# Kernel tuning notes

Hardware: AMD Instinct MI355X
Metric: run time of the kernel (lower is better)

## Reference

```python
import jax, jax.numpy as jnp
import numpy as np

N_NODES = 100000
N_EDGES = 1600000
IN_DIM = 128
HID_DIM = 128
OUT_DIM = 2


def sage_conv(x, src, dst, deg_inv, W_l, W_r, b):
    # mean-aggregate neighbor features: messages flow src -> dst
    agg = jax.ops.segment_sum(x[src], dst, num_segments=N_NODES)  # [N, d_in]
    agg = agg * deg_inv[:, None]
    # PyG SAGEConv: out = lin_l(aggr) + lin_r(x); bias only on lin_l
    return agg @ W_l + x @ W_r + b


def setup_inputs() -> dict:
    key = jax.random.key(0)
    ks = jax.random.split(key, 9)
    x = jax.random.normal(ks[0], (N_NODES, IN_DIM), dtype=jnp.float32)
    edge_index = jax.random.randint(ks[1], (2, N_EDGES), 0, N_NODES, dtype=jnp.int64)

    def glorot(k, shape):
        lim = float(np.sqrt(6.0 / (shape[0] + shape[1])))
        return jax.random.uniform(k, shape, jnp.float32, -lim, lim)

    return {
        "x": x,
        "edge_index": edge_index,
        "W1_l": glorot(ks[2], (IN_DIM, HID_DIM)),
        "W1_r": glorot(ks[3], (IN_DIM, HID_DIM)),
        "b1": jnp.zeros((HID_DIM,), jnp.float32),
        "W2_l": glorot(ks[4], (HID_DIM, HID_DIM)),
        "W2_r": glorot(ks[5], (HID_DIM, HID_DIM)),
        "b2": jnp.zeros((HID_DIM,), jnp.float32),
        "W3_l": glorot(ks[6], (HID_DIM, OUT_DIM)),
        "W3_r": glorot(ks[7], (HID_DIM, OUT_DIM)),
        "b3": jnp.zeros((OUT_DIM,), jnp.float32),
    }


def reference(x, edge_index, W1_l, W1_r, b1, W2_l, W2_r, b2, W3_l, W3_r, b3):
    src, dst = edge_index[0], edge_index[1]
    # mean-aggregation normalization: 1/in-degree (clamped to >=1)
    deg = jax.ops.segment_sum(jnp.ones((N_EDGES,), jnp.float32), dst, num_segments=N_NODES)
    deg_inv = 1.0 / jnp.maximum(deg, 1.0)

    h = sage_conv(x, src, dst, deg_inv, W1_l, W1_r, b1)
    h = jax.nn.relu(h)  # dropout is identity in eval mode
    h = sage_conv(h, src, dst, deg_inv, W2_l, W2_r, b2)
    h = jax.nn.relu(h)
    h = sage_conv(h, src, dst, deg_inv, W3_l, W3_r, b3)
    h = jax.nn.relu(h)
    return jax.nn.log_softmax(h, axis=1)
```

## Files before the change

### kernel.cpp

```cpp
#include <hip/hip_runtime.h>
#include <math.h>

#define DIM 128

typedef __attribute__((ext_vector_type(8))) short bf16x8;
typedef __attribute__((ext_vector_type(4))) float f32x4;

__device__ __forceinline__ ushort f2bf(float f) {
  unsigned u = __float_as_uint(f);
  return (ushort)((u + 0x7FFFu + ((u >> 16) & 1u)) >> 16);
}
__device__ __forceinline__ float bf2f(ushort h) {
  return __uint_as_float(((unsigned)h) << 16);
}


__global__ __launch_bounds__(256) void count_cast_kernel(
    const int* __restrict__ dst, unsigned* __restrict__ counts, int E, int NB, int NBUCK,
    const float* __restrict__ x, ushort* __restrict__ xh, long total_f,
    const float* __restrict__ W1l, const float* __restrict__ W1r,
    const float* __restrict__ W2l, const float* __restrict__ W2r,
    ushort* __restrict__ tabs, int CB) {
  __shared__ unsigned hist[1024];
  const int tid = threadIdx.x;
  int bid = blockIdx.x;
  if (bid < NB) {
    for (int i = tid; i < NBUCK; i += 256) hist[i] = 0u;
    __syncthreads();
    long base = (long)bid * 2048;
#pragma unroll
    for (int c = 0; c < 8; ++c) {
      long e = base + c * 256 + tid;
      if (e < E) atomicAdd(&hist[((unsigned)dst[e]) >> 7], 1u);
    }
    __syncthreads();
    for (int i = tid; i < NBUCK; i += 256)
      counts[(size_t)bid * NBUCK + i] = hist[i];
    return;
  }
  int aid = bid - NB;
  if (aid < CB) {
    long i = ((long)aid * 2048 + tid) * 4;
    for (int c = 0; c < 8; ++c, i += 1024) {
      if (i >= total_f) break;
      float4 v = *(const float4*)(x + i);
      uint2 Hh;
      Hh.x = (unsigned)f2bf(v.x) | ((unsigned)f2bf(v.y) << 16);
      Hh.y = (unsigned)f2bf(v.z) | ((unsigned)f2bf(v.w) << 16);
      *(uint2*)(xh + i) = Hh;
    }
    return;
  }
  int aid2 = aid - CB;
  if (aid2 < 256) {
    int m = aid2 >> 6;
    const float* W = (m == 0) ? W1l : (m == 1) ? W1r : (m == 2) ? W2l : W2r;
    ushort* Ht = tabs + (size_t)m * 16384;
    int idx = (aid2 & 63) * 256 + tid;
    int k = idx >> 7, n = idx & 127;
    Ht[n * DIM + k] = f2bf(W[idx]);
  }
}

__global__ __launch_bounds__(256) void colscan_kernel(unsigned* __restrict__ counts,
                                                      unsigned* __restrict__ totals,
                                                      int NB, int NBUCK) {
  int wid = (blockIdx.x << 2) + (threadIdx.x >> 6);
  int lane = threadIdx.x & 63;
  if (wid >= NBUCK) return;
  unsigned carry = 0u;
  for (int k0 = 0; k0 < NB; k0 += 64) {
    int k = k0 + lane;
    unsigned v = (k < NB) ? counts[(size_t)k * NBUCK + wid] : 0u;
    unsigned s = v;
#pragma unroll
    for (int o = 1; o < 64; o <<= 1) {
      unsigned t = __shfl_up(s, o, 64);
      if (lane >= o) s += t;
    }
    if (k < NB) counts[(size_t)k * NBUCK + wid] = carry + s - v;
    carry += __shfl(s, 63, 64);
  }
  if (lane == 0) totals[wid] = carry;
}

__global__ __launch_bounds__(256) void totscan_kernel(unsigned* __restrict__ totals,
                                                      int NBUCK, int E) {
  __shared__ unsigned s[256];
  __shared__ unsigned carry;
  if (threadIdx.x == 0) carry = 0u;
  __syncthreads();
  for (int base = 0; base < NBUCK; base += 256) {
    int i = base + threadIdx.x;
    unsigned v = (i < NBUCK) ? totals[i] : 0u;
    s[threadIdx.x] = v;
    __syncthreads();
#pragma unroll
    for (int d = 1; d < 256; d <<= 1) {
      unsigned t = (threadIdx.x >= d) ? s[threadIdx.x - d] : 0u;
      __syncthreads();
      s[threadIdx.x] += t;
      __syncthreads();
    }
    if (i < NBUCK) totals[i] = carry + s[threadIdx.x] - v;
    __syncthreads();
    if (threadIdx.x == 0) carry += s[255];
    __syncthreads();
  }
  if (threadIdx.x == 0) totals[NBUCK] = (unsigned)E;
}

__global__ __launch_bounds__(256) void cscatter_kernel(
    const int* __restrict__ src, const int* __restrict__ dst,
    const unsigned* __restrict__ counts, const unsigned* __restrict__ totals,
    uint2* __restrict__ pairs, int E, int NBUCK) {
  __shared__ unsigned basec[1024];
  const int tid = threadIdx.x;
  const int bid = blockIdx.x;
  for (int i = tid; i < NBUCK; i += 256)
    basec[i] = counts[(size_t)bid * NBUCK + i] + totals[i];
  __syncthreads();
  long base = (long)bid * 2048;
#pragma unroll
  for (int c = 0; c < 8; ++c) {
    long e = base + c * 256 + tid;
    if (e < E) {
      int d = dst[e];
      unsigned pos = atomicAdd(&basec[((unsigned)d) >> 7], 1u);
      pairs[pos] = make_uint2((unsigned)src[e], (unsigned)d);
    }
  }
}

__global__ __launch_bounds__(256) void fine_kernel(
    const uint2* __restrict__ pairs, const unsigned* __restrict__ totals,
    int* __restrict__ csr_src, unsigned* __restrict__ offs, float* __restrict__ dinv,
    int N, int NBUCK, int E) {
  __shared__ int lsrc[4096];
  __shared__ ushort ldst[4096];
  __shared__ unsigned hist[128], excl[128], cur[128];
  const int tid = threadIdx.x;
  const int b = blockIdx.x;
  const unsigned t0 = totals[b], t1 = totals[b + 1];
  unsigned cnt = t1 - t0;
  if (cnt > 4096u) cnt = 4096u;
  if (tid < 128) { hist[tid] = 0u; cur[tid] = 0u; }
  __syncthreads();
  for (unsigned i = tid; i < cnt; i += 256) {
    uint2 p = pairs[t0 + i];
    lsrc[i] = (int)p.x;
    int nl = (int)(p.y & 127u);
    ldst[i] = (ushort)nl;
    atomicAdd(&hist[nl], 1u);
  }
  __syncthreads();
  if (tid < 64) {
    unsigned v0 = hist[tid], v1 = hist[tid + 64];
    unsigned s0 = v0, s1 = v1;
#pragma unroll
    for (int o = 1; o < 64; o <<= 1) {
      unsigned u0 = __shfl_up(s0, o, 64);
      unsigned u1 = __shfl_up(s1, o, 64);
      if (tid >= o) { s0 += u0; s1 += u1; }
    }
    unsigned tot0 = __shfl(s0, 63, 64);
    excl[tid] = s0 - v0;
    excl[tid + 64] = tot0 + s1 - v1;
  }
  __syncthreads();
  if (tid < 128) {
    int node = (b << 7) + tid;
    if (node < N) {
      offs[node] = t0 + excl[tid];
      dinv[node] = 1.0f / fmaxf((float)hist[tid], 1.0f);
    }
  }
  if (b == 0 && tid == 255) offs[N] = (unsigned)E;
  for (unsigned i = tid; i < cnt; i += 256) {
    int nl = (int)ldst[i];
    unsigned slot = excl[nl] + atomicAdd(&cur[nl], 1u);
    csr_src[t0 + slot] = lsrc[i];
  }
}


#define GATHER_BODY(TABLE)                                                       \
  const int node = (blockIdx.x * 256 + threadIdx.x) >> 6;                        \
  if (node >= N) return;                                                         \
  const int lane = threadIdx.x & 63;                                             \
  const int eslot = lane >> 4;                                                   \
  const int col = lane & 15;                                                     \
  const unsigned beg = off[node], end = off[node + 1];                           \
  const ushort* fbase = (TABLE) + col * 8;                                       \
  float acc[8];                                                                  \
  _Pragma("unroll") for (int t = 0; t < 8; ++t) acc[t] = 0.f;                    \
  auto accum = [&](int4 v) {                                                     \
    unsigned w0 = (unsigned)v.x, w1 = (unsigned)v.y;                             \
    unsigned w2 = (unsigned)v.z, w3 = (unsigned)v.w;                             \
    acc[0] += __uint_as_float(w0 << 16);                                         \
    acc[1] += __uint_as_float(w0 & 0xFFFF0000u);                                 \
    acc[2] += __uint_as_float(w1 << 16);                                         \
    acc[3] += __uint_as_float(w1 & 0xFFFF0000u);                                 \
    acc[4] += __uint_as_float(w2 << 16);                                         \
    acc[5] += __uint_as_float(w2 & 0xFFFF0000u);                                 \
    acc[6] += __uint_as_float(w3 << 16);                                         \
    acc[7] += __uint_as_float(w3 & 0xFFFF0000u);                                 \
  };                                                                             \
  unsigned base = beg;                                                           \
  for (; base + 16 <= end; base += 16) {                                         \
    int s0 = csr_src[base + eslot];                                              \
    int s1 = csr_src[base + 4 + eslot];                                          \
    int s2 = csr_src[base + 8 + eslot];                                          \
    int s3 = csr_src[base + 12 + eslot];                                         \
    int4 v0 = *(const int4*)(fbase + (size_t)s0 * DIM);                          \
    int4 v1 = *(const int4*)(fbase + (size_t)s1 * DIM);                          \
    int4 v2 = *(const int4*)(fbase + (size_t)s2 * DIM);                          \
    int4 v3 = *(const int4*)(fbase + (size_t)s3 * DIM);                          \
    accum(v0); accum(v1); accum(v2); accum(v3);                                  \
  }                                                                              \
  for (; base + 8 <= end; base += 8) {                                           \
    int s0 = csr_src[base + eslot];                                              \
    int s1 = csr_src[base + 4 + eslot];                                          \
    int4 v0 = *(const int4*)(fbase + (size_t)s0 * DIM);                          \
    int4 v1 = *(const int4*)(fbase + (size_t)s1 * DIM);                          \
    accum(v0); accum(v1);                                                        \
  }                                                                              \
  for (unsigned e = base + eslot; e < end; e += 4) {                             \
    int s = csr_src[e];                                                          \
    int4 v = *(const int4*)(fbase + (size_t)s * DIM);                            \
    accum(v);                                                                    \
  }                                                                              \
  _Pragma("unroll") for (int t = 0; t < 8; ++t) {                                \
    acc[t] += __shfl_xor(acc[t], 32, 64);                                        \
    acc[t] += __shfl_xor(acc[t], 16, 64);                                        \
  }

__global__ __launch_bounds__(256) void gather_wave_kernel(
    const ushort* __restrict__ featH, const int* __restrict__ csr_src,
    const unsigned* __restrict__ off, const float* __restrict__ dinv,
    ushort* __restrict__ aggH, int N) {
  GATHER_BODY(featH)
  if (eslot == 0) {
    float di = dinv[node];
    unsigned ph[4];
#pragma unroll
    for (int t = 0; t < 4; ++t) {
      ph[t] = (unsigned)f2bf(acc[2 * t] * di) | ((unsigned)f2bf(acc[2 * t + 1] * di) << 16);
    }
    *(int4*)(aggH + (size_t)node * DIM + col * 8) =
        make_int4((int)ph[0], (int)ph[1], (int)ph[2], (int)ph[3]);
  }
}

__global__ __launch_bounds__(256) void sage_mfma_kernel(
    const ushort* __restrict__ aggH, const ushort* xH,
    const ushort* __restrict__ WlH, const ushort* __restrict__ WrH,
    const float* __restrict__ bias,
    const float* __restrict__ W3l, const float* __restrict__ W3r,
    ushort* __restrict__ outH, float* __restrict__ y, int N) {
  __shared__ ushort As[128 * 64];
  __shared__ ushort Bs[128 * 64];

  const int tid = threadIdx.x;
  const int bm = blockIdx.x * 128;
  const int wave = tid >> 6;
  const int lane = tid & 63;
  const int l15 = lane & 15;
  const int quad = lane >> 4;
  const int wm = wave >> 1;
  const int wn = wave & 1;

  f32x4 acc[4][4];
#pragma unroll
  for (int i = 0; i < 4; ++i)
#pragma unroll
    for (int j = 0; j < 4; ++j) acc[i][j] = (f32x4){0.f, 0.f, 0.f, 0.f};

  for (int g = 0; g < 4; ++g) {
    const ushort* Ap = (g < 2) ? aggH : xH;
    const ushort* Wp = (g < 2) ? WlH : WrH;
    const int kt = (g & 1) << 6;
    __syncthreads();
#pragma unroll
    for (int c = 0; c < 4; ++c) {
      int flat = c * 256 + tid;
      int row = flat >> 3;
      int kg = flat & 7;
      int swz = (kg ^ (row & 7)) << 3;
      int grow = bm + row;
      if (grow >= N) grow = N - 1;
      *(int4*)(&As[row * 64 + swz]) = *(const int4*)(Ap + (size_t)grow * DIM + kt + kg * 8);
      *(int4*)(&Bs[row * 64 + swz]) = *(const int4*)(Wp + (size_t)row * DIM + kt + kg * 8);
    }
    __syncthreads();
#pragma unroll
    for (int ks = 0; ks < 2; ++ks) {
      bf16x8 af[4], bfr[4];
      int kg = (ks << 2) + quad;
#pragma unroll
      for (int i = 0; i < 4; ++i) {
        int ar = (wm << 6) + (i << 4) + l15;
        af[i] = *(const bf16x8*)(&As[ar * 64 + ((kg ^ (ar & 7)) << 3)]);
        int br = (wn << 6) + (i << 4) + l15;
        bfr[i] = *(const bf16x8*)(&Bs[br * 64 + ((kg ^ (br & 7)) << 3)]);
      }
#pragma unroll
      for (int i = 0; i < 4; ++i)
#pragma unroll
        for (int j = 0; j < 4; ++j)
          acc[i][j] = __builtin_amdgcn_mfma_f32_16x16x32_bf16(af[i], bfr[j], acc[i][j], 0, 0, 0);
    }
  }

  __syncthreads();
  float* WcF = reinterpret_cast<float*>(As);
  float* YpF = reinterpret_cast<float*>(As) + 512;

  if (W3l) {
    for (int t = tid; t < 512; t += 256) {
      int col = t >> 2, c = t & 3;
      WcF[t] = (c < 2) ? W3l[col * 2 + c] : W3r[col * 2 + (c - 2)];
    }
    __syncthreads();
  }

  float bv[4];
#pragma unroll
  for (int j = 0; j < 4; ++j) bv[j] = bias[(wn << 6) + (j << 4) + l15];

#pragma unroll
  for (int i = 0; i < 4; ++i) {
#pragma unroll
    for (int r = 0; r < 4; ++r) {
      const int rowl = (wm << 6) + (i << 4) + (quad << 2) + r;
      const int grow = bm + rowl;
      float p0 = 0.f, p1 = 0.f, p2 = 0.f, p3 = 0.f;
#pragma unroll
      for (int j = 0; j < 4; ++j) {
        int col = (wn << 6) + (j << 4) + l15;
        float v = fmaxf(acc[i][j][r] + bv[j], 0.f);
        ushort h = f2bf(v);
        if (outH && grow < N) outH[(size_t)grow * DIM + col] = h;
        if (W3l) {
          float qv = bf2f(h);
          p0 += qv * WcF[col * 4 + 0];
          p1 += qv * WcF[col * 4 + 1];
          p2 += qv * WcF[col * 4 + 2];
          p3 += qv * WcF[col * 4 + 3];
        }
      }
      if (W3l) {
#pragma unroll
        for (int o = 1; o < 16; o <<= 1) {
          p0 += __shfl_xor(p0, o, 64);
          p1 += __shfl_xor(p1, o, 64);
          p2 += __shfl_xor(p2, o, 64);
          p3 += __shfl_xor(p3, o, 64);
        }
        if (l15 == 0) {
          YpF[(rowl * 4 + 0) * 2 + wn] = p0;
          YpF[(rowl * 4 + 1) * 2 + wn] = p1;
          YpF[(rowl * 4 + 2) * 2 + wn] = p2;
          YpF[(rowl * 4 + 3) * 2 + wn] = p3;
        }
      }
    }
  }

  if (W3l) {
    __syncthreads();
    for (int t = tid; t < 512; t += 256) {
      int grow = bm + (t >> 2);
      if (grow < N) y[(size_t)grow * 4 + (t & 3)] = YpF[t * 2 + 0] + YpF[t * 2 + 1];
    }
  }
}

__global__ __launch_bounds__(256) void final3_kernel(const float* __restrict__ y,
                                                     const int* __restrict__ csr_src,
                                                     const unsigned* __restrict__ off,
                                                     const float* __restrict__ dinv,
                                                     const float* __restrict__ b3,
                                                     float* __restrict__ out, int N) {
  int n = blockIdx.x * 256 + threadIdx.x;
  if (n >= N) return;
  unsigned beg = off[n], end = off[n + 1];
  float s0 = 0.f, s1 = 0.f;
  for (unsigned e = beg; e < end; ++e) {
    int s = csr_src[e];
    float2 v = *reinterpret_cast<const float2*>(&y[(size_t)s * 4]);
    s0 += v.x; s1 += v.y;
  }
  float di = dinv[n];
  float o0 = fmaxf(s0 * di + y[(size_t)n * 4 + 2] + b3[0], 0.f);
  float o1 = fmaxf(s1 * di + y[(size_t)n * 4 + 3] + b3[1], 0.f);
  float m = fmaxf(o0, o1);
  float l = m + logf(expf(o0 - m) + expf(o1 - m));
  out[n * 2 + 0] = o0 - l;
  out[n * 2 + 1] = o1 - l;
}

extern "C" void kernel_launch(void* const* d_in, const int* in_sizes, int n_in,
                              void* d_out, int out_size, void* d_ws, size_t ws_size,
                              hipStream_t stream) {
  const float* x   = (const float*)d_in[0];
  const int*   ei  = (const int*)d_in[1];
  const float* W1l = (const float*)d_in[2];
  const float* W1r = (const float*)d_in[3];
  const float* b1  = (const float*)d_in[4];
  const float* W2l = (const float*)d_in[5];
  const float* W2r = (const float*)d_in[6];
  const float* b2  = (const float*)d_in[7];
  const float* W3l = (const float*)d_in[8];
  const float* W3r = (const float*)d_in[9];
  const float* b3  = (const float*)d_in[10];

  const int N = in_sizes[0] / DIM;
  const int E = in_sizes[1] / 2;
  const int* src = ei;
  const int* dst = ei + E;

  const int NBUCK = (N + 127) >> 7;
  const int NB    = (E + 2047) / 2048;
  const long total_f = (long)N * DIM;
  const int CB    = (int)((total_f / 4 + 2047) / 2048);

  char* ws = (char*)d_ws;
  size_t off_b = 0;
  auto alloc = [&](size_t bytes) {
    void* p = ws + off_b;
    off_b = (off_b + bytes + 255) & ~(size_t)255;
    return p;
  };
  unsigned* counts  = (unsigned*)alloc((size_t)NB * NBUCK * 4);
  unsigned* totals  = (unsigned*)alloc((size_t)(NBUCK + 1) * 4);
  void*     shared_ = alloc((size_t)N * DIM * 2);
  uint2*    pairs   = (uint2*)shared_;
  ushort*   aggH    = (ushort*)shared_;
  int*      csr_src = (int*)alloc((size_t)E * 4);
  unsigned* offs    = (unsigned*)alloc((size_t)(N + 1) * 4);
  float*    dinv    = (float*)alloc((size_t)N * 4);
  ushort*   xh      = (ushort*)alloc((size_t)N * DIM * 2);
  ushort*   tabs    = (ushort*)alloc((size_t)4 * 16384 * 2);
  float*    y       = (float*)alloc((size_t)N * 4 * 4);

  count_cast_kernel<<<NB + CB + 256, 256, 0, stream>>>(
      dst, counts, E, NB, NBUCK, x, xh, total_f, W1l, W1r, W2l, W2r, tabs, CB);
  colscan_kernel<<<(NBUCK + 3) / 4, 256, 0, stream>>>(counts, totals, NB, NBUCK);
  totscan_kernel<<<1, 256, 0, stream>>>(totals, NBUCK, E);
  cscatter_kernel<<<NB, 256, 0, stream>>>(src, dst, counts, totals, pairs, E, NBUCK);
  fine_kernel<<<NBUCK, 256, 0, stream>>>(pairs, totals, csr_src, offs, dinv, N, NBUCK, E);

  const ushort* W1lH = tabs;
  const ushort* W1rH = tabs + 16384;
  const ushort* W2lH = tabs + 32768;
  const ushort* W2rH = tabs + 49152;
  const int G = (N + 127) / 128;
  const int gather_grid = (N + 3) / 4;

  gather_wave_kernel<<<gather_grid, 256, 0, stream>>>(xh, csr_src, offs, dinv, aggH, N);
  sage_mfma_kernel<<<G, 256, 0, stream>>>(aggH, xh, W1lH, W1rH, b1,
                                          nullptr, nullptr, xh, nullptr, N);
  gather_wave_kernel<<<gather_grid, 256, 0, stream>>>(xh, csr_src, offs, dinv, aggH, N);
  sage_mfma_kernel<<<G, 256, 0, stream>>>(aggH, xh, W2lH, W2rH, b2,
                                          W3l, W3r, nullptr, y, N);
  final3_kernel<<<(N + 255) / 256, 256, 0, stream>>>(y, csr_src, offs, dinv, b3, (float*)d_out, N);
}
```

Before: 360.4 us.

## Reorder layer-2 as transform-then-aggregate, fuse W3 projection into gather

Layer 2 now runs the GEMMs first: a dual-output MFMA kernel computes h@W2_l and h@W2_r+b2. A new gather kernel then aggregates the pre-transformed features, applies ReLU and projects onto W3, which removes the separate aggregate-then-GEMM pass and the W3 epilogue in the MFMA kernel. Edge pairs are also packed into 32 bits (src<<7 | local dst), and the gather tail is made branchless with clamped loads. The layer-1 MFMA epilogue now stages output through LDS so global stores are coalesced. The cost is an extra N×128 bf16 buffer and rounding h@W2_l to bf16 before aggregation, which slightly changes numerics.

```diff
diff --git a/kernel.cpp b/kernel.cpp
--- a/kernel.cpp
+++ b/kernel.cpp
@@ -113,7 +113,7 @@
 __global__ __launch_bounds__(256) void cscatter_kernel(
     const int* __restrict__ src, const int* __restrict__ dst,
     const unsigned* __restrict__ counts, const unsigned* __restrict__ totals,
-    uint2* __restrict__ pairs, int E, int NBUCK) {
+    unsigned* __restrict__ pairs, int E, int NBUCK) {
   __shared__ unsigned basec[1024];
   const int tid = threadIdx.x;
   const int bid = blockIdx.x;
@@ -125,15 +125,15 @@
   for (int c = 0; c < 8; ++c) {
     long e = base + c * 256 + tid;
     if (e < E) {
-      int d = dst[e];
-      unsigned pos = atomicAdd(&basec[((unsigned)d) >> 7], 1u);
-      pairs[pos] = make_uint2((unsigned)src[e], (unsigned)d);
+      unsigned d = (unsigned)dst[e];
+      unsigned pos = atomicAdd(&basec[d >> 7], 1u);
+      pairs[pos] = ((unsigned)src[e] << 7) | (d & 127u);
     }
   }
 }
 
 __global__ __launch_bounds__(256) void fine_kernel(
-    const uint2* __restrict__ pairs, const unsigned* __restrict__ totals,
+    const unsigned* __restrict__ pairs, const unsigned* __restrict__ totals,
     int* __restrict__ csr_src, unsigned* __restrict__ offs, float* __restrict__ dinv,
     int N, int NBUCK, int E) {
   __shared__ int lsrc[4096];
@@ -147,9 +147,9 @@
   if (tid < 128) { hist[tid] = 0u; cur[tid] = 0u; }
   __syncthreads();
   for (unsigned i = tid; i < cnt; i += 256) {
-    uint2 p = pairs[t0 + i];
-    lsrc[i] = (int)p.x;
-    int nl = (int)(p.y & 127u);
+    unsigned p = pairs[t0 + i];
+    lsrc[i] = (int)(p >> 7);
+    int nl = (int)(p & 127u);
     ldst[i] = (ushort)nl;
     atomicAdd(&hist[nl], 1u);
   }
@@ -218,17 +218,21 @@
     int4 v3 = *(const int4*)(fbase + (size_t)s3 * DIM);                          \
     accum(v0); accum(v1); accum(v2); accum(v3);                                  \
   }                                                                              \
-  for (; base + 8 <= end; base += 8) {                                           \
-    int s0 = csr_src[base + eslot];                                              \
-    int s1 = csr_src[base + 4 + eslot];                                          \
+  if (base < end) {                                                              \
+    unsigned e0 = base + eslot, e1 = base + 4 + eslot;                           \
+    unsigned e2 = base + 8 + eslot, e3 = base + 12 + eslot;                      \
+    int s0 = csr_src[e0 < end ? e0 : end - 1];                                   \
+    int s1 = csr_src[e1 < end ? e1 : end - 1];                                   \
+    int s2 = csr_src[e2 < end ? e2 : end - 1];                                   \
+    int s3 = csr_src[e3 < end ? e3 : end - 1];                                   \
     int4 v0 = *(const int4*)(fbase + (size_t)s0 * DIM);                          \
     int4 v1 = *(const int4*)(fbase + (size_t)s1 * DIM);                          \
-    accum(v0); accum(v1);                                                        \
-  }                                                                              \
-  for (unsigned e = base + eslot; e < end; e += 4) {                             \
-    int s = csr_src[e];                                                          \
-    int4 v = *(const int4*)(fbase + (size_t)s * DIM);                            \
-    accum(v);                                                                    \
+    int4 v2 = *(const int4*)(fbase + (size_t)s2 * DIM);                          \
+    int4 v3 = *(const int4*)(fbase + (size_t)s3 * DIM);                          \
+    if (e0 < end) accum(v0);                                                     \
+    if (e1 < end) accum(v1);                                                     \
+    if (e2 < end) accum(v2);                                                     \
+    if (e3 < end) accum(v3);                                                     \
   }                                                                              \
   _Pragma("unroll") for (int t = 0; t < 8; ++t) {                                \
     acc[t] += __shfl_xor(acc[t], 32, 64);                                        \
@@ -252,12 +256,52 @@
   }
 }
 
+__global__ __launch_bounds__(256) void gather2_kernel(
+    const ushort* __restrict__ h1l, const int* __restrict__ csr_src,
+    const unsigned* __restrict__ off, const float* __restrict__ dinv,
+    const ushort* __restrict__ h1r, const float* __restrict__ W3l,
+    const float* __restrict__ W3r, float* __restrict__ y, int N) {
+  GATHER_BODY(h1l)
+  if (eslot == 0) {
+    float di = dinv[node];
+    int4 xv = *(const int4*)(h1r + (size_t)node * DIM + col * 8);
+    unsigned w0 = (unsigned)xv.x, w1 = (unsigned)xv.y;
+    unsigned w2 = (unsigned)xv.z, w3 = (unsigned)xv.w;
+    float h[8];
+    h[0] = fmaxf(acc[0] * di + __uint_as_float(w0 << 16), 0.f);
+    h[1] = fmaxf(acc[1] * di + __uint_as_float(w0 & 0xFFFF0000u), 0.f);
+    h[2] = fmaxf(acc[2] * di + __uint_as_float(w1 << 16), 0.f);
+    h[3] = fmaxf(acc[3] * di + __uint_as_float(w1 & 0xFFFF0000u), 0.f);
+    h[4] = fmaxf(acc[4] * di + __uint_as_float(w2 << 16), 0.f);
+    h[5] = fmaxf(acc[5] * di + __uint_as_float(w2 & 0xFFFF0000u), 0.f);
+    h[6] = fmaxf(acc[6] * di + __uint_as_float(w3 << 16), 0.f);
+    h[7] = fmaxf(acc[7] * di + __uint_as_float(w3 & 0xFFFF0000u), 0.f);
+    const int d0 = col * 8;
+    float y0 = 0.f, y1 = 0.f, y2 = 0.f, y3 = 0.f;
+#pragma unroll
+    for (int t = 0; t < 8; t += 2) {
+      float4 wl = *(const float4*)(W3l + (size_t)(d0 + t) * 2);
+      float4 wr = *(const float4*)(W3r + (size_t)(d0 + t) * 2);
+      y0 += h[t] * wl.x + h[t + 1] * wl.z;
+      y1 += h[t] * wl.y + h[t + 1] * wl.w;
+      y2 += h[t] * wr.x + h[t + 1] * wr.z;
+      y3 += h[t] * wr.y + h[t + 1] * wr.w;
+    }
+#pragma unroll
+    for (int o = 1; o < 16; o <<= 1) {
+      y0 += __shfl_xor(y0, o, 64);
+      y1 += __shfl_xor(y1, o, 64);
+      y2 += __shfl_xor(y2, o, 64);
+      y3 += __shfl_xor(y3, o, 64);
+    }
+    if (lane == 0) *(float4*)(y + (size_t)node * 4) = make_float4(y0, y1, y2, y3);
+  }
+}
+
 __global__ __launch_bounds__(256) void sage_mfma_kernel(
     const ushort* __restrict__ aggH, const ushort* xH,
     const ushort* __restrict__ WlH, const ushort* __restrict__ WrH,
-    const float* __restrict__ bias,
-    const float* __restrict__ W3l, const float* __restrict__ W3r,
-    ushort* __restrict__ outH, float* __restrict__ y, int N) {
+    const float* __restrict__ bias, ushort* __restrict__ outH, int N) {
   __shared__ ushort As[128 * 64];
   __shared__ ushort Bs[128 * 64];
 
@@ -312,66 +356,125 @@
     }
   }
 
-  __syncthreads();
-  float* WcF = reinterpret_cast<float*>(As);
-  float* YpF = reinterpret_cast<float*>(As) + 512;
-
-  if (W3l) {
-    for (int t = tid; t < 512; t += 256) {
-      int col = t >> 2, c = t & 3;
-      WcF[t] = (c < 2) ? W3l[col * 2 + c] : W3r[col * 2 + (c - 2)];
-    }
-    __syncthreads();
-  }
-
   float bv[4];
 #pragma unroll
   for (int j = 0; j < 4; ++j) bv[j] = bias[(wn << 6) + (j << 4) + l15];
 
-#pragma unroll
-  for (int i = 0; i < 4; ++i) {
-#pragma unroll
-    for (int r = 0; r < 4; ++r) {
-      const int rowl = (wm << 6) + (i << 4) + (quad << 2) + r;
-      const int grow = bm + rowl;
-      float p0 = 0.f, p1 = 0.f, p2 = 0.f, p3 = 0.f;
-#pragma unroll
-      for (int j = 0; j < 4; ++j) {
-        int col = (wn << 6) + (j << 4) + l15;
-        float v = fmaxf(acc[i][j][r] + bv[j], 0.f);
-        ushort h = f2bf(v);
-        if (outH && grow < N) outH[(size_t)grow * DIM + col] = h;
-        if (W3l) {
-          float qv = bf2f(h);
-          p0 += qv * WcF[col * 4 + 0];
-          p1 += qv * WcF[col * 4 + 1];
-          p2 += qv * WcF[col * 4 + 2];
-          p3 += qv * WcF[col * 4 + 3];
+  __syncthreads();
+#pragma unroll
+  for (int i = 0; i < 4; ++i)
+#pragma unroll
+    for (int j = 0; j < 4; ++j)
+#pragma unroll
+      for (int r = 0; r < 4; ++r) {
+        int row = (wm << 6) + (i << 4) + (quad << 2) + r;
+        int colc = (wn << 6) + (j << 4) + l15;
+        ((ushort*)As)[((row & 63) << 7) + colc + ((row >> 6) << 13)] =
+            f2bf(fmaxf(acc[i][j][r] + bv[j], 0.f));
+      }
+  __syncthreads();
+#pragma unroll
+  for (int c = 0; c < 8; ++c) {
+    int flat = c * 256 + tid;
+    int row = flat >> 4;
+    int grow = bm + row;
+    if (grow < N)
+      *(int4*)(outH + (size_t)grow * DIM + (flat & 15) * 8) =
+          *(const int4*)((const ushort*)As + flat * 8);
+  }
+}
+
+__global__ __launch_bounds__(256) void gemm2_dual_kernel(
+    const ushort* __restrict__ h1, const ushort* __restrict__ tabs2,
+    const float* __restrict__ b2, ushort* __restrict__ h1l, ushort* __restrict__ h1r, int N) {
+  __shared__ ushort L[3 * 128 * 64];
+  ushort* As = L;
+  ushort* Bs0 = L + 8192;
+  ushort* Bs1 = L + 16384;
+  const int tid = threadIdx.x;
+  const int bm = blockIdx.x * 128;
+  const int wave = tid >> 6;
+  const int lane = tid & 63;
+  const int l15 = lane & 15;
+  const int quad = lane >> 4;
+  const int wm = wave >> 1;
+  const int wn = wave & 1;
+
+  f32x4 accl[4][4], accr[4][4];
+#pragma unroll
+  for (int i = 0; i < 4; ++i)
+#pragma unroll
+    for (int j = 0; j < 4; ++j) {
+      accl[i][j] = (f32x4){0.f, 0.f, 0.f, 0.f};
+      accr[i][j] = (f32x4){0.f, 0.f, 0.f, 0.f};
+    }
+
+  for (int g = 0; g < 2; ++g) {
+    const int kt = g << 6;
+    __syncthreads();
+#pragma unroll
+    for (int c = 0; c < 4; ++c) {
+      int flat = c * 256 + tid;
+      int row = flat >> 3;
+      int kg = flat & 7;
+      int swz = (kg ^ (row & 7)) << 3;
+      int grow = bm + row;
+      if (grow >= N) grow = N - 1;
+      *(int4*)(&As[row * 64 + swz]) = *(const int4*)(h1 + (size_t)grow * DIM + kt + kg * 8);
+      *(int4*)(&Bs0[row * 64 + swz]) = *(const int4*)(tabs2 + (size_t)row * DIM + kt + kg * 8);
+      *(int4*)(&Bs1[row * 64 + swz]) =
+          *(const int4*)(tabs2 + 16384 + (size_t)row * DIM + kt + kg * 8);
+    }
+    __syncthreads();
+#pragma unroll
+    for (int ks = 0; ks < 2; ++ks) {
+      bf16x8 af[4], bl[4], br[4];
+      int kg = (ks << 2) + quad;
+#pragma unroll
+      for (int i = 0; i < 4; ++i) {
+        int ar = (wm << 6) + (i << 4) + l15;
+        af[i] = *(const bf16x8*)(&As[ar * 64 + ((kg ^ (ar & 7)) << 3)]);
+        int nr = (wn << 6) + (i << 4) + l15;
+        bl[i] = *(const bf16x8*)(&Bs0[nr * 64 + ((kg ^ (nr & 7)) << 3)]);
+        br[i] = *(const bf16x8*)(&Bs1[nr * 64 + ((kg ^ (nr & 7)) << 3)]);
+      }
+#pragma unroll
+      for (int i = 0; i < 4; ++i)
+#pragma unroll
+        for (int j = 0; j < 4; ++j) {
+          accl[i][j] = __builtin_amdgcn_mfma_f32_16x16x32_bf16(af[i], bl[j], accl[i][j], 0, 0, 0);
+          accr[i][j] = __builtin_amdgcn_mfma_f32_16x16x32_bf16(af[i], br[j], accr[i][j], 0, 0, 0);
         }
-      }
-      if (W3l) {
-#pragma unroll
-        for (int o = 1; o < 16; o <<= 1) {
-          p0 += __shfl_xor(p0, o, 64);
-          p1 += __shfl_xor(p1, o, 64);
-          p2 += __shfl_xor(p2, o, 64);
-          p3 += __shfl_xor(p3, o, 64);
+    }
+  }
+
+  float bv[4];
+#pragma unroll
+  for (int j = 0; j < 4; ++j) bv[j] = b2[(wn << 6) + (j << 4) + l15];
+
+#pragma unroll
+  for (int m = 0; m < 2; ++m) {
+    __syncthreads();
+#pragma unroll
+    for (int i = 0; i < 4; ++i)
+#pragma unroll
+      for (int j = 0; j < 4; ++j)
+#pragma unroll
+        for (int r = 0; r < 4; ++r) {
+          int row = (wm << 6) + (i << 4) + (quad << 2) + r;
+          int colc = (wn << 6) + (j << 4) + l15;
+          float v = m ? (accr[i][j][r] + bv[j]) : accl[i][j][r];
+          L[row * 128 + colc] = f2bf(v);
         }
-        if (l15 == 0) {
-          YpF[(rowl * 4 + 0) * 2 + wn] = p0;
-          YpF[(rowl * 4 + 1) * 2 + wn] = p1;
-          YpF[(rowl * 4 + 2) * 2 + wn] = p2;
-          YpF[(rowl * 4 + 3) * 2 + wn] = p3;
-        }
-      }
-    }
-  }
-
-  if (W3l) {
-    __syncthreads();
-    for (int t = tid; t < 512; t += 256) {
-      int grow = bm + (t >> 2);
-      if (grow < N) y[(size_t)grow * 4 + (t & 3)] = YpF[t * 2 + 0] + YpF[t * 2 + 1];
+    __syncthreads();
+    ushort* out = m ? h1r : h1l;
+#pragma unroll
+    for (int c = 0; c < 8; ++c) {
+      int flat = c * 256 + tid;
+      int row = flat >> 4;
+      int grow = bm + row;
+      if (grow < N)
+        *(int4*)(out + (size_t)grow * DIM + (flat & 15) * 8) = *(const int4*)(&L[flat * 8]);
     }
   }
 }
@@ -435,14 +538,16 @@
   unsigned* counts  = (unsigned*)alloc((size_t)NB * NBUCK * 4);
   unsigned* totals  = (unsigned*)alloc((size_t)(NBUCK + 1) * 4);
   void*     shared_ = alloc((size_t)N * DIM * 2);
-  uint2*    pairs   = (uint2*)shared_;
+  unsigned* pairs   = (unsigned*)shared_;
   ushort*   aggH    = (ushort*)shared_;
+  ushort*   h1l     = (ushort*)shared_;
   int*      csr_src = (int*)alloc((size_t)E * 4);
   unsigned* offs    = (unsigned*)alloc((size_t)(N + 1) * 4);
   float*    dinv    = (float*)alloc((size_t)N * 4);
   ushort*   xh      = (ushort*)alloc((size_t)N * DIM * 2);
   ushort*   tabs    = (ushort*)alloc((size_t)4 * 16384 * 2);
   float*    y       = (float*)alloc((size_t)N * 4 * 4);
+  ushort*   h1r     = (ushort*)alloc((size_t)N * DIM * 2);
 
   count_cast_kernel<<<NB + CB + 256, 256, 0, stream>>>(
       dst, counts, E, NB, NBUCK, x, xh, total_f, W1l, W1r, W2l, W2r, tabs, CB);
@@ -453,16 +558,13 @@
 
   const ushort* W1lH = tabs;
   const ushort* W1rH = tabs + 16384;
-  const ushort* W2lH = tabs + 32768;
-  const ushort* W2rH = tabs + 49152;
+  const ushort* tabs2 = tabs + 32768;
   const int G = (N + 127) / 128;
   const int gather_grid = (N + 3) / 4;
 
   gather_wave_kernel<<<gather_grid, 256, 0, stream>>>(xh, csr_src, offs, dinv, aggH, N);
-  sage_mfma_kernel<<<G, 256, 0, stream>>>(aggH, xh, W1lH, W1rH, b1,
-                                          nullptr, nullptr, xh, nullptr, N);
-  gather_wave_kernel<<<gather_grid, 256, 0, stream>>>(xh, csr_src, offs, dinv, aggH, N);
-  sage_mfma_kernel<<<G, 256, 0, stream>>>(aggH, xh, W2lH, W2rH, b2,
-                                          W3l, W3r, nullptr, y, N);
+  sage_mfma_kernel<<<G, 256, 0, stream>>>(aggH, xh, W1lH, W1rH, b1, xh, N);
+  gemm2_dual_kernel<<<G, 256, 0, stream>>>(xh, tabs2, b2, h1l, h1r, N);
+  gather2_kernel<<<gather_grid, 256, 0, stream>>>(h1l, csr_src, offs, dinv, h1r, W3l, W3r, y, N);
   final3_kernel<<<(N + 255) / 256, 256, 0, stream>>>(y, csr_src, offs, dinv, b3, (float*)d_out, N);
 }
```

Measured after the change: 353.7 us. About the same (-1.9%).
